# Optimization experiments

Measured on AMD Instinct MI355X. Metric: run time of the kernel, lower is better.

## Reference

```python
import jax, jax.numpy as jnp
import numpy as np

K = 9
SIGMA = 4.0
RADIUS = 16  # round(4*sigma)
IMAGE_SHAPE = (256, 256)


def _gaussian_kernel_1d():
    i = jnp.arange(2 * RADIUS + 1, dtype=jnp.float32) - RADIUS
    g = jnp.exp(-(i ** 2) / (2.0 * SIGMA ** 2))
    return g / jnp.sum(g)


def _gaussian_blur(x):
    # x: [b, H, W, 1]; separable Gaussian blur, reflect-101 borders (cv2 default)
    g = _gaussian_kernel_1d()
    xp = jnp.pad(x, ((0, 0), (RADIUS, RADIUS), (RADIUS, RADIUS), (0, 0)), mode='reflect')
    dn = ('NHWC', 'HWIO', 'NHWC')
    kv = g.reshape(2 * RADIUS + 1, 1, 1, 1)  # vertical pass
    kh = g.reshape(1, 2 * RADIUS + 1, 1, 1)  # horizontal pass
    y = jax.lax.conv_general_dilated(xp, kv, (1, 1), 'VALID', dimension_numbers=dn)
    y = jax.lax.conv_general_dilated(y, kh, (1, 1), 'VALID', dimension_numbers=dn)
    return y


def setup_inputs() -> dict:
    key = jax.random.key(0)
    k1, k2 = jax.random.split(key)
    inputs = jax.random.normal(k1, (8, 32, 32, 512), dtype=jnp.float32)
    feature_vector = jax.random.normal(k2, (16384, 512), dtype=jnp.float32)
    return {"inputs": inputs, "feature_vector": feature_vector}


def reference(inputs, feature_vector):
    b, h, w, c = inputs.shape
    feat = inputs.reshape(b * h * w, c)
    # pairwise euclidean distances: [b*h*w, N]
    d2 = (jnp.sum(feat ** 2, axis=-1, keepdims=True)
          + jnp.sum(feature_vector ** 2, axis=-1)[None, :]
          - 2.0 * feat @ feature_vector.T)
    dist = jnp.sqrt(jnp.maximum(d2, 0.0))
    # k smallest distances, ascending (equivalent to tf.sort(...)[..., :k])
    neg_topk, _ = jax.lax.top_k(-dist, K)
    score = -neg_topk  # [b*h*w, K], ascending
    mask = score[:, 0].reshape(b, h, w, 1)
    score = score.reshape(b, h * w, K)
    # patch with maximal nearest-neighbor distance
    idx = jnp.argmax(score[..., 0], axis=-1)  # [b]
    conf = jnp.take_along_axis(score, idx[:, None, None], axis=1)[:, 0, :]  # [b, K]
    exp_conf = jnp.exp(conf)
    weight = 1.0 - jnp.max(exp_conf, axis=-1) / jnp.sum(exp_conf, axis=-1)
    score_out = (jnp.max(score[..., 0], axis=-1) * weight)[:, None]  # [b, 1]
    mask = jax.image.resize(mask, (b, *IMAGE_SHAPE, 1), method='bilinear', antialias=False)
    mask = _gaussian_blur(mask)
    return score_out, mask
```

## Files before the change

kernel.cpp:

```cpp
#include <hip/hip_runtime.h>

typedef __attribute__((ext_vector_type(8))) short bf16x8;
typedef __attribute__((ext_vector_type(4))) float f32x4;

static constexpr int M = 8192;
static constexpr int N = 16384;
static constexpr int K = 512;
static constexpr int BM = 128;
static constexpr int BN = 128;
static constexpr int BK = 64;
static constexpr int KCHUNKS = K / BK;
static constexpr int NGROUPS_S = 8;
static constexpr int GROUP_N_S = N / NGROUPS_S;
static constexpr int NTILES_S = GROUP_N_S / BN;
static constexpr int NGROUPS_F = 16;
static constexpr int GROUP_N_F = N / NGROUPS_F;
static constexpr int NTILES_F = GROUP_N_F / BN;
static constexpr int NCHUNK = NTILES_F * KCHUNKS;
static constexpr float F_INF = 3.0e38f;

__device__ __forceinline__ unsigned short f2bf(float f) {
    unsigned int u = __float_as_uint(f);
    return (unsigned short)((u + 0x7fffu + ((u >> 16) & 1u)) >> 16);
}

__device__ __forceinline__ void gl_lds16(const unsigned short* g, unsigned short* l) {
    __builtin_amdgcn_global_load_lds(
        (const __attribute__((address_space(1))) unsigned int*)g,
        (__attribute__((address_space(3))) unsigned int*)l, 16, 0, 0);
}

__global__ void k_prep(const float* __restrict__ Q, const float* __restrict__ F,
                       unsigned short* __restrict__ Qb, unsigned short* __restrict__ Fb,
                       float* __restrict__ qn, float* __restrict__ fn) {
    int wid = blockIdx.x * 4 + (threadIdx.x >> 6);
    int lane = threadIdx.x & 63;
    bool isQ = wid < M;
    const float* src = isQ ? (Q + (size_t)wid * K) : (F + (size_t)(wid - M) * K);
    unsigned short* dst = isQ ? (Qb + (size_t)wid * K) : (Fb + (size_t)(wid - M) * K);
    const float4* p = reinterpret_cast<const float4*>(src) + lane * 2;
    float4 a = p[0], b = p[1];
    float s = a.x*a.x + a.y*a.y + a.z*a.z + a.w*a.w
            + b.x*b.x + b.y*b.y + b.z*b.z + b.w*b.w;
    bf16x8 v;
    v[0]=(short)f2bf(a.x); v[1]=(short)f2bf(a.y); v[2]=(short)f2bf(a.z); v[3]=(short)f2bf(a.w);
    v[4]=(short)f2bf(b.x); v[5]=(short)f2bf(b.y); v[6]=(short)f2bf(b.z); v[7]=(short)f2bf(b.w);
    *reinterpret_cast<bf16x8*>(dst + lane * 8) = v;
    #pragma unroll
    for (int d = 1; d < 64; d <<= 1) s += __shfl_xor(s, d);
    if (lane == 0) { if (isQ) qn[wid] = s; else fn[wid - M] = s; }
}

__global__ void k_norms(const float* __restrict__ Q, const float* __restrict__ F,
                        float* __restrict__ qn, float* __restrict__ fn) {
    int wid = blockIdx.x * 4 + (threadIdx.x >> 6);
    int lane = threadIdx.x & 63;
    const float* src = (wid < M) ? (Q + (size_t)wid * K) : (F + (size_t)(wid - M) * K);
    const float4* p = reinterpret_cast<const float4*>(src) + lane * 2;
    float4 a = p[0], b = p[1];
    float s = a.x*a.x + a.y*a.y + a.z*a.z + a.w*a.w
            + b.x*b.x + b.y*b.y + b.z*b.z + b.w*b.w;
    #pragma unroll
    for (int d = 1; d < 64; d <<= 1) s += __shfl_xor(s, d);
    if (lane == 0) { if (wid < M) qn[wid] = s; else fn[wid - M] = s; }
}

__global__ __launch_bounds__(256, 2)
void k_mingemm2(const unsigned short* __restrict__ Qb, const unsigned short* __restrict__ Fb,
                const float* __restrict__ qn, const float* __restrict__ fn,
                float* __restrict__ pv, unsigned int* __restrict__ pi) {
    __shared__ unsigned short As[2][BM * BK];
    __shared__ unsigned short Bs[2][BN * BK];
    __shared__ float qn_t[BM];
    __shared__ float fn_g[GROUP_N_F];

    const int tid = threadIdx.x;
    const int lane = tid & 63;
    const int wave = tid >> 6;
    const int wr = wave >> 1, wc = wave & 1;
    const int l15 = lane & 15, l4 = lane >> 4;

    const int wg = blockIdx.x;
    const int swz = (wg & 7) * 128 + (wg >> 3);
    const int group = swz >> 6;
    const int rowblk = swz & 63;
    const int row0 = rowblk * BM;
    const int gbase = group * GROUP_N_F;

    const int r_l = lane >> 3, p8 = lane & 7;
    const int g8 = p8 ^ r_l;
    const unsigned short* gA[4];
    const unsigned short* gB[4];
    #pragma unroll
    for (int i = 0; i < 4; ++i) {
        int row = (wave * 4 + i) * 8 + r_l;
        gA[i] = Qb + (size_t)(row0 + row) * K + g8 * 8;
        gB[i] = Fb + (size_t)(gbase + row) * K + g8 * 8;
    }

    auto stage = [&](int ct, int buf) {
        const int kc = ct & 7;
        const size_t bo = (size_t)(ct >> 3) * BN * K;
        #pragma unroll
        for (int i = 0; i < 4; ++i) gl_lds16(gA[i] + kc * BK, &As[buf][(wave * 4 + i) * 512]);
        #pragma unroll
        for (int i = 0; i < 4; ++i) gl_lds16(gB[i] + bo + kc * BK, &Bs[buf][(wave * 4 + i) * 512]);
    };

    for (int i = tid; i < GROUP_N_F; i += 256) fn_g[i] = fn[gbase + i];
    if (tid < BM) qn_t[tid] = qn[row0 + tid];
    stage(0, 0);
    __syncthreads();

    float qnv[4][4];
    #pragma unroll
    for (int fi = 0; fi < 4; ++fi)
        #pragma unroll
        for (int j = 0; j < 4; ++j)
            qnv[fi][j] = qn_t[wr*64 + fi*16 + l4*4 + j];

    float mval[4][4];
    unsigned int midx[4][4];
    #pragma unroll
    for (int a = 0; a < 4; ++a)
        #pragma unroll
        for (int b = 0; b < 4; ++b) { mval[a][b] = F_INF; midx[a][b] = 0; }

    int cur = 0;
    for (int nt = 0; nt < NTILES_F; ++nt) {
        f32x4 acc[4][4];
        #pragma unroll
        for (int a = 0; a < 4; ++a)
            #pragma unroll
            for (int b = 0; b < 4; ++b) acc[a][b] = f32x4{0.f, 0.f, 0.f, 0.f};

        for (int kc = 0; kc < KCHUNKS; ++kc) {
            const int ct = nt * KCHUNKS + kc;
            if (ct + 1 < NCHUNK) {
                stage(ct + 1, cur ^ 1);
                asm volatile("s_waitcnt vmcnt(8)" ::: "memory");
            } else {
                asm volatile("s_waitcnt vmcnt(0)" ::: "memory");
            }
            __builtin_amdgcn_sched_barrier(0);
            __builtin_amdgcn_s_barrier();
            #pragma unroll
            for (int ks = 0; ks < 2; ++ks) {
                const int gidx = ks * 4 + l4;
                bf16x8 af[4], bfv[4];
                #pragma unroll
                for (int fi = 0; fi < 4; ++fi) {
                    int r = wr*64 + fi*16 + l15;
                    int pg = gidx ^ (r & 7);
                    af[fi] = *reinterpret_cast<const bf16x8*>(&As[cur][r*BK + pg*8]);
                }
                #pragma unroll
                for (int fj = 0; fj < 4; ++fj) {
                    int r = wc*64 + fj*16 + l15;
                    int pg = gidx ^ (r & 7);
                    bfv[fj] = *reinterpret_cast<const bf16x8*>(&Bs[cur][r*BK + pg*8]);
                }
                #pragma unroll
                for (int fi = 0; fi < 4; ++fi)
                    #pragma unroll
                    for (int fj = 0; fj < 4; ++fj)
                        acc[fi][fj] = __builtin_amdgcn_mfma_f32_16x16x32_bf16(
                            af[fi], bfv[fj], acc[fi][fj], 0, 0, 0);
            }
            __builtin_amdgcn_sched_barrier(0);
            __builtin_amdgcn_s_barrier();
            cur ^= 1;
        }
        const int colb = gbase + nt * BN + wc * 64;
        float fnv[4];
        #pragma unroll
        for (int fj = 0; fj < 4; ++fj) fnv[fj] = fn_g[nt*BN + wc*64 + fj*16 + l15];
        #pragma unroll
        for (int fi = 0; fi < 4; ++fi) {
            #pragma unroll
            for (int j = 0; j < 4; ++j) {
                float qv = qnv[fi][j];
                #pragma unroll
                for (int fj = 0; fj < 4; ++fj) {
                    float d2 = qv + fnv[fj] - 2.0f * acc[fi][fj][j];
                    if (d2 < mval[fi][j]) {
                        mval[fi][j] = d2;
                        midx[fi][j] = (unsigned int)(colb + fj*16 + l15);
                    }
                }
            }
        }
    }
    #pragma unroll
    for (int fi = 0; fi < 4; ++fi) {
        #pragma unroll
        for (int j = 0; j < 4; ++j) {
            float v = mval[fi][j];
            unsigned int ix = midx[fi][j];
            #pragma unroll
            for (int d = 1; d < 16; d <<= 1) {
                float ov = __shfl_xor(v, d);
                unsigned int oi = (unsigned int)__shfl_xor((int)ix, d);
                if (ov < v) { v = ov; ix = oi; }
            }
            if (l15 == 0) {
                int rg = row0 + wr*64 + fi*16 + l4*4 + j;
                int pidx = rg * 32 + group*2 + wc;
                pv[pidx] = v;
                pi[pidx] = ix;
            }
        }
    }
}

__global__ __launch_bounds__(256, 2)
void k_mingemm_cast(const float* __restrict__ Q, const float* __restrict__ F,
                    const float* __restrict__ qn, const float* __restrict__ fn,
                    float* __restrict__ pv, unsigned int* __restrict__ pi) {
    __shared__ unsigned short As[BM * BK];
    __shared__ unsigned short Bs[BN * BK];
    __shared__ float qn_t[BM];
    __shared__ float fn_t[BN];

    const int tid = threadIdx.x;
    const int lane = tid & 63;
    const int wave = tid >> 6;
    const int wr = wave >> 1, wc = wave & 1;
    const int l15 = lane & 15, l4 = lane >> 4;

    const int row0 = blockIdx.x * BM;
    const int gbase = blockIdx.y * GROUP_N_S;

    const int srow = tid >> 3;
    const int p8 = tid & 7;
    const int g8 = p8 ^ (srow & 7);
    const float* pA[4];
    const float* pB[4];
    int dstOff[4];
    #pragma unroll
    for (int i = 0; i < 4; ++i) {
        int r = i * 32 + srow;
        pA[i] = Q + (size_t)(row0 + r) * K + g8 * 8;
        pB[i] = F + (size_t)(gbase + r) * K + g8 * 8;
        dstOff[i] = r * BK + p8 * 8;
    }

    float mval[4][4];
    unsigned int midx[4][4];
    float qnv[4][4];
    #pragma unroll
    for (int a = 0; a < 4; ++a)
        #pragma unroll
        for (int b = 0; b < 4; ++b) { mval[a][b] = F_INF; midx[a][b] = 0; qnv[a][b] = 0.f; }

    for (int nt = 0; nt < NTILES_S; ++nt) {
        f32x4 acc[4][4];
        #pragma unroll
        for (int a = 0; a < 4; ++a)
            #pragma unroll
            for (int b = 0; b < 4; ++b) acc[a][b] = f32x4{0.f, 0.f, 0.f, 0.f};

        for (int kc = 0; kc < KCHUNKS; ++kc) {
            __syncthreads();
            #pragma unroll
            for (int i = 0; i < 4; ++i) {
                const float4* sa = reinterpret_cast<const float4*>(pA[i] + kc * BK);
                float4 xa = sa[0], ya = sa[1];
                const float4* sb = reinterpret_cast<const float4*>(pB[i] + nt * (BN * K) + kc * BK);
                float4 xb = sb[0], yb = sb[1];
                bf16x8 va, vb;
                va[0]=(short)f2bf(xa.x); va[1]=(short)f2bf(xa.y); va[2]=(short)f2bf(xa.z); va[3]=(short)f2bf(xa.w);
                va[4]=(short)f2bf(ya.x); va[5]=(short)f2bf(ya.y); va[6]=(short)f2bf(ya.z); va[7]=(short)f2bf(ya.w);
                vb[0]=(short)f2bf(xb.x); vb[1]=(short)f2bf(xb.y); vb[2]=(short)f2bf(xb.z); vb[3]=(short)f2bf(xb.w);
                vb[4]=(short)f2bf(yb.x); vb[5]=(short)f2bf(yb.y); vb[6]=(short)f2bf(yb.z); vb[7]=(short)f2bf(yb.w);
                *reinterpret_cast<bf16x8*>(&As[dstOff[i]]) = va;
                *reinterpret_cast<bf16x8*>(&Bs[dstOff[i]]) = vb;
            }
            if (kc == 0) {
                if (nt == 0 && tid < BM) qn_t[tid] = qn[row0 + tid];
                if (tid < BN) fn_t[tid] = fn[gbase + nt * BN + tid];
            }
            __syncthreads();
            if (nt == 0 && kc == 0) {
                #pragma unroll
                for (int fi = 0; fi < 4; ++fi)
                    #pragma unroll
                    for (int j = 0; j < 4; ++j)
                        qnv[fi][j] = qn_t[wr*64 + fi*16 + l4*4 + j];
            }
            #pragma unroll
            for (int ks = 0; ks < 2; ++ks) {
                const int gidx = ks * 4 + l4;
                bf16x8 af[4], bfv[4];
                #pragma unroll
                for (int fi = 0; fi < 4; ++fi) {
                    int r = wr*64 + fi*16 + l15;
                    int pg = gidx ^ (r & 7);
                    af[fi] = *reinterpret_cast<const bf16x8*>(&As[r*BK + pg*8]);
                }
                #pragma unroll
                for (int fj = 0; fj < 4; ++fj) {
                    int r = wc*64 + fj*16 + l15;
                    int pg = gidx ^ (r & 7);
                    bfv[fj] = *reinterpret_cast<const bf16x8*>(&Bs[r*BK + pg*8]);
                }
                #pragma unroll
                for (int fi = 0; fi < 4; ++fi)
                    #pragma unroll
                    for (int fj = 0; fj < 4; ++fj)
                        acc[fi][fj] = __builtin_amdgcn_mfma_f32_16x16x32_bf16(
                            af[fi], bfv[fj], acc[fi][fj], 0, 0, 0);
            }
        }
        const int colb = gbase + nt * BN + wc * 64;
        float fnv[4];
        #pragma unroll
        for (int fj = 0; fj < 4; ++fj) fnv[fj] = fn_t[wc*64 + fj*16 + l15];
        #pragma unroll
        for (int fi = 0; fi < 4; ++fi) {
            #pragma unroll
            for (int j = 0; j < 4; ++j) {
                float qv = qnv[fi][j];
                #pragma unroll
                for (int fj = 0; fj < 4; ++fj) {
                    float d2 = qv + fnv[fj] - 2.0f * acc[fi][fj][j];
                    if (d2 < mval[fi][j]) {
                        mval[fi][j] = d2;
                        midx[fi][j] = (unsigned int)(colb + fj*16 + l15);
                    }
                }
            }
        }
    }
    #pragma unroll
    for (int fi = 0; fi < 4; ++fi) {
        #pragma unroll
        for (int j = 0; j < 4; ++j) {
            float v = mval[fi][j];
            unsigned int ix = midx[fi][j];
            #pragma unroll
            for (int d = 1; d < 16; d <<= 1) {
                float ov = __shfl_xor(v, d);
                unsigned int oi = (unsigned int)__shfl_xor((int)ix, d);
                if (ov < v) { v = ov; ix = oi; }
            }
            if (l15 == 0) {
                int rg = row0 + wr*64 + fi*16 + l4*4 + j;
                int pidx = rg * 16 + blockIdx.y * 2 + wc;
                pv[pidx] = v;
                pi[pidx] = ix;
            }
        }
    }
}

__global__ void k_refine(const float* __restrict__ Q, const float* __restrict__ F,
                         const float* __restrict__ pv, const unsigned int* __restrict__ pi,
                         float* __restrict__ minD, int PS) {
    int row = blockIdx.x * 4 + (threadIdx.x >> 6);
    int lane = threadIdx.x & 63;
    float v = F_INF; unsigned int ix = 0;
    if (lane < PS) { v = pv[row*PS + lane]; ix = pi[row*PS + lane]; }
    #pragma unroll
    for (int d = 1; d < 64; d <<= 1) {
        float ov = __shfl_xor(v, d);
        unsigned int oi = (unsigned int)__shfl_xor((int)ix, d);
        if (ov < v) { v = ov; ix = oi; }
    }
    const float4* q = reinterpret_cast<const float4*>(Q + (size_t)row * K) + lane*2;
    const float4* f = reinterpret_cast<const float4*>(F + (size_t)ix * K) + lane*2;
    float4 a0 = q[0], a1 = q[1], b0 = f[0], b1 = f[1];
    float s = 0.f, dx;
    dx = a0.x-b0.x; s += dx*dx;  dx = a0.y-b0.y; s += dx*dx;
    dx = a0.z-b0.z; s += dx*dx;  dx = a0.w-b0.w; s += dx*dx;
    dx = a1.x-b1.x; s += dx*dx;  dx = a1.y-b1.y; s += dx*dx;
    dx = a1.z-b1.z; s += dx*dx;  dx = a1.w-b1.w; s += dx*dx;
    #pragma unroll
    for (int d = 1; d < 64; d <<= 1) s += __shfl_xor(s, d);
    if (lane == 0) minD[row] = sqrtf(s);
}

__global__ void k_argmax(const float* __restrict__ minD, unsigned int* __restrict__ sel) {
    __shared__ float sv[256];
    __shared__ int si[256];
    int b = blockIdx.x, tid = threadIdx.x;
    float bv = -F_INF; int bi = 0;
    for (int p = tid; p < 1024; p += 256) {
        float v = minD[b*1024 + p];
        if (v > bv) { bv = v; bi = p; }
    }
    sv[tid] = bv; si[tid] = bi;
    __syncthreads();
    for (int s = 128; s > 0; s >>= 1) {
        if (tid < s) {
            if (sv[tid+s] > sv[tid] || (sv[tid+s] == sv[tid] && si[tid+s] < si[tid])) {
                sv[tid] = sv[tid+s]; si[tid] = si[tid+s];
            }
        }
        __syncthreads();
    }
    if (tid == 0) sel[b] = (unsigned int)(b*1024 + si[0]);
}

__global__ void k_dist8(const float* __restrict__ Q, const float* __restrict__ F,
                        const unsigned int* __restrict__ sel, float* __restrict__ d2all) {
    __shared__ float qs[8][512];
    int tid = threadIdx.x;
    int lane = tid & 63, wave = tid >> 6;
    for (int i = tid; i < 8*512; i += 256) {
        int b = i >> 9;
        qs[b][i & 511] = Q[(size_t)sel[b] * K + (i & 511)];
    }
    __syncthreads();
    int base = blockIdx.x * 128 + wave * 32;
    for (int r = 0; r < 32; ++r) {
        int row = base + r;
        const float4* fp = reinterpret_cast<const float4*>(F + (size_t)row * K) + lane*2;
        float4 f0 = fp[0], f1 = fp[1];
        float fv[8] = {f0.x,f0.y,f0.z,f0.w,f1.x,f1.y,f1.z,f1.w};
        float accb[8];
        #pragma unroll
        for (int b = 0; b < 8; ++b) {
            float s = 0.f;
            #pragma unroll
            for (int e = 0; e < 8; ++e) {
                float d = fv[e] - qs[b][lane*8 + e];
                s += d * d;
            }
            accb[b] = s;
        }
        #pragma unroll
        for (int d = 1; d < 64; d <<= 1)
            #pragma unroll
            for (int b = 0; b < 8; ++b) accb[b] += __shfl_xor(accb[b], d);
        if (lane == 0) {
            #pragma unroll
            for (int b = 0; b < 8; ++b) d2all[b * N + row] = accb[b];
        }
    }
}

__global__ void k_sel9(const float* __restrict__ d2all, float* __restrict__ out) {
    __shared__ float sv[256 * 10];
    int b = blockIdx.x, tid = threadIdx.x;
    float v[9];
    #pragma unroll
    for (int i = 0; i < 9; ++i) v[i] = F_INF;
    for (int i = tid; i < N; i += 256) {
        float x = d2all[b * N + i];
        #pragma unroll
        for (int s = 0; s < 9; ++s) {
            float lo = fminf(v[s], x), hi = fmaxf(v[s], x);
            v[s] = lo; x = hi;
        }
    }
    #pragma unroll
    for (int i = 0; i < 9; ++i) sv[tid*10 + i] = v[i];
    sv[tid*10 + 9] = F_INF;
    __syncthreads();
    for (int s = 128; s > 0; s >>= 1) {
        if (tid < s) {
            int ia = 1, ib = 1;
            float av = sv[tid*10], bv = sv[(tid+s)*10];
            float c[9];
            #pragma unroll
            for (int k = 0; k < 9; ++k) {
                bool ta = av <= bv;
                c[k] = ta ? av : bv;
                float na = sv[tid*10 + ia], nb = sv[(tid+s)*10 + ib];
                if (ta) { av = na; ++ia; } else { bv = nb; ++ib; }
            }
            #pragma unroll
            for (int k = 0; k < 9; ++k) sv[tid*10 + k] = c[k];
        }
        __syncthreads();
    }
    if (tid == 0) {
        float c[9];
        #pragma unroll
        for (int i = 0; i < 9; ++i) c[i] = sqrtf(fmaxf(sv[i], 0.f));
        float S = 0.f;
        #pragma unroll
        for (int i = 0; i < 9; ++i) S += expf(c[i] - c[8]);
        out[b] = c[0] * (1.f - 1.f / S);
    }
}

__global__ void k_top9(const float* __restrict__ Q, const float* __restrict__ F,
                       const unsigned int* __restrict__ sel, float* __restrict__ part9) {
    __shared__ float qs[512];
    __shared__ float dist[2048];
    __shared__ float rv[256];
    __shared__ int ri[256];
    int b = blockIdx.x >> 3, g = blockIdx.x & 7;
    int tid = threadIdx.x;
    unsigned int srow = sel[b];
    if (tid < 128)
        reinterpret_cast<float4*>(qs)[tid] =
            reinterpret_cast<const float4*>(Q + (size_t)srow * K)[tid];
    __syncthreads();
    #pragma unroll
    for (int e = 0; e < 8; ++e) {
        int fl = tid + 256*e;
        const float* fp = F + (size_t)(g*2048 + fl) * K;
        float s = 0.f;
        for (int k = 0; k < 512; k += 4) {
            float4 fv4 = *reinterpret_cast<const float4*>(fp + k);
            float d0 = qs[k]   - fv4.x;
            float d1 = qs[k+1] - fv4.y;
            float d2 = qs[k+2] - fv4.z;
            float d3 = qs[k+3] - fv4.w;
            s += d0*d0 + d1*d1 + d2*d2 + d3*d3;
        }
        dist[fl] = s;
    }
    __syncthreads();
    for (int it = 0; it < 9; ++it) {
        float lv = F_INF; int li = 0;
        #pragma unroll
        for (int e = 0; e < 8; ++e) {
            int idx = tid + 256*e;
            float v = dist[idx];
            if (v < lv) { lv = v; li = idx; }
        }
        rv[tid] = lv; ri[tid] = li;
        __syncthreads();
        for (int s = 128; s > 0; s >>= 1) {
            if (tid < s && rv[tid+s] < rv[tid]) { rv[tid] = rv[tid+s]; ri[tid] = ri[tid+s]; }
            __syncthreads();
        }
        if (tid == 0) {
            part9[(b*8+g)*9 + it] = rv[0];
            dist[ri[0]] = F_INF;
        }
        __syncthreads();
    }
}

__global__ void k_final(const float* __restrict__ part9, float* __restrict__ out) {
    int b = threadIdx.x;
    if (b >= 8) return;
    float arr[9];
    #pragma unroll
    for (int i = 0; i < 9; ++i) arr[i] = F_INF;
    for (int g = 0; g < 8; ++g)
        for (int i = 0; i < 9; ++i) {
            float v = part9[(b*8+g)*9 + i];
            #pragma unroll
            for (int s = 0; s < 9; ++s) {
                float lo = fminf(arr[s], v), hi = fmaxf(arr[s], v);
                arr[s] = lo; v = hi;
            }
        }
    float c[9];
    #pragma unroll
    for (int i = 0; i < 9; ++i) c[i] = sqrtf(fmaxf(arr[i], 0.f));
    float c8 = c[8], S = 0.f;
    #pragma unroll
    for (int i = 0; i < 9; ++i) S += expf(c[i] - c8);
    float w = 1.f - 1.f / S;
    out[b] = c[0] * w;
}

__global__ void k_wmat(float* __restrict__ W) {
    int idx = blockIdx.x * 256 + threadIdx.x;
    int o = idx >> 5, j = idx & 31;
    float gsum = 0.f;
    #pragma unroll
    for (int u = 0; u < 33; ++u) { float d = (float)(u - 16); gsum += expf(-d*d * (1.f/32.f)); }
    float acc = 0.f;
    for (int u = 0; u < 33; ++u) {
        float d = (float)(u - 16);
        float gu = expf(-d*d * (1.f/32.f));
        int y = o + u - 16;
        y = y < 0 ? -y : (y > 255 ? 510 - y : y);
        float xin = ((float)y + 0.5f) * 0.125f - 0.5f;
        float j0f = floorf(xin);
        int j0 = (int)j0f;
        float wfr = xin - j0f;
        float r;
        if (j0 < 0) r = (j == 0) ? 1.f : 0.f;
        else if (j0 >= 31) r = (j == 31) ? 1.f : 0.f;
        else r = (j == j0) ? (1.f - wfr) : ((j == j0 + 1) ? wfr : 0.f);
        acc += gu * r;
    }
    W[idx] = acc / gsum;
}

__global__ void k_mask(const float* __restrict__ minD, const float* __restrict__ W,
                       float* __restrict__ outm) {
    __shared__ float Ms[1024];
    __shared__ float Ws[8192];
    __shared__ float Ts[8192];
    int b = blockIdx.x, tid = threadIdx.x;
    for (int i = tid; i < 1024; i += 256) Ms[i] = minD[b*1024 + i];
    for (int i = tid; i < 8192; i += 256) Ws[i] = W[i];
    __syncthreads();
    {
        int o = tid;
        float wrow[32];
        #pragma unroll
        for (int i = 0; i < 32; ++i) wrow[i] = Ws[o*32 + i];
        for (int j = 0; j < 32; ++j) {
            float s = 0.f;
            #pragma unroll
            for (int i = 0; i < 32; ++i) s += wrow[i] * Ms[i*32 + j];
            Ts[o*32 + j] = s;
        }
    }
    __syncthreads();
    {
        int p = tid;
        float wp[32];
        #pragma unroll
        for (int j = 0; j < 32; ++j) wp[j] = Ws[p*32 + j];
        float* dst = outm + (size_t)b * 65536;
        for (int o = 0; o < 256; ++o) {
            float s = 0.f;
            #pragma unroll
            for (int j = 0; j < 32; ++j) s += Ts[o*32 + j] * wp[j];
            dst[o*256 + p] = s;
        }
    }
}

extern "C" void kernel_launch(void* const* d_in, const int* in_sizes, int n_in,
                              void* d_out, int out_size, void* d_ws, size_t ws_size,
                              hipStream_t stream) {
    const float* Q = (const float*)d_in[0];
    const float* F = (const float*)d_in[1];
    float* out = (float*)d_out;

    const size_t smallFloats = (size_t)8192*32*2 + 8192 + 8 + 576 + (size_t)8*N + 8192 + 16384 + 8192;
    const size_t REQ = smallFloats*4 + (size_t)M*K*2 + (size_t)N*K*2;
    const bool fast = ws_size >= REQ;
    const int PS = fast ? 32 : 16;

    float* ws = (float*)d_ws;
    float* pv = ws;
    unsigned int* pi = (unsigned int*)(pv + 8192*PS);
    float* minD = (float*)(pi + 8192*PS);
    unsigned int* sel = (unsigned int*)(minD + 8192);
    float* part9 = (float*)(sel + 8);
    float* d2all = part9 + 576;
    float* qn = d2all + (size_t)8*N;
    float* fn = qn + 8192;
    float* W  = fn + 16384;
    unsigned short* Qb = (unsigned short*)(W + 8192);
    unsigned short* Fb = Qb + (size_t)M*K;

    k_wmat <<<dim3(32), 256, 0, stream>>>(W);
    if (fast) {
        k_prep <<<dim3((M + N) / 4), 256, 0, stream>>>(Q, F, Qb, Fb, qn, fn);
        k_mingemm2<<<dim3(M / BM * NGROUPS_F), 256, 0, stream>>>(Qb, Fb, qn, fn, pv, pi);
        k_refine<<<dim3(M / 4), 256, 0, stream>>>(Q, F, pv, pi, minD, PS);
        k_argmax<<<dim3(8), 256, 0, stream>>>(minD, sel);
        k_dist8<<<dim3(N / 128), 256, 0, stream>>>(Q, F, sel, d2all);
        k_sel9 <<<dim3(8), 256, 0, stream>>>(d2all, out);
    } else {
        k_norms<<<dim3((M + N) / 4), 256, 0, stream>>>(Q, F, qn, fn);
        k_mingemm_cast<<<dim3(M / BM, NGROUPS_S), 256, 0, stream>>>(Q, F, qn, fn, pv, pi);
        k_refine<<<dim3(M / 4), 256, 0, stream>>>(Q, F, pv, pi, minD, PS);
        k_argmax<<<dim3(8), 256, 0, stream>>>(minD, sel);
        k_top9 <<<dim3(64), 256, 0, stream>>>(Q, F, sel, part9);
        k_final<<<dim3(1), 64, 0, stream>>>(part9, out);
    }
    k_mask <<<dim3(8), 256, 0, stream>>>(minD, W, out + 8);
}
```

Measured before the change: 346.4 us.

## Replace min-GEMM with 256x256 output-tile kernel using 8 waves and interleaved LDS loads

The fast path's min-distance GEMM moves from 128x128 tiles that each loop over a group of N columns to one 256x256 output tile per workgroup with 512 threads. Each workgroup covers a single column block and writes a per-row partial min for it, so there are 64 partials per row and k_refine reads all of them. Inside the kernel, MFMAs on the first half of the A fragments are interleaved with LDS reads of the second half and with the global-to-LDS prefetch, and s_setprio raises priority around the MFMA bursts. The aim is more arithmetic per byte staged and better overlap of memory with compute, at the cost of more registers, a larger partial-min buffer and a cross-wave reduction through LDS.

```diff
diff --git a/kernel.cpp b/kernel.cpp
--- a/kernel.cpp
+++ b/kernel.cpp
@@ -6,17 +6,17 @@
 static constexpr int M = 8192;
 static constexpr int N = 16384;
 static constexpr int K = 512;
-static constexpr int BM = 128;
-static constexpr int BN = 128;
+static constexpr int BM = 256;
+static constexpr int BN = 256;
 static constexpr int BK = 64;
 static constexpr int KCHUNKS = K / BK;
+static constexpr int RBLK = M / BM;
+static constexpr int CBLK = N / BN;
+static constexpr int BMs = 128;
+static constexpr int BKs = 64;
 static constexpr int NGROUPS_S = 8;
 static constexpr int GROUP_N_S = N / NGROUPS_S;
-static constexpr int NTILES_S = GROUP_N_S / BN;
-static constexpr int NGROUPS_F = 16;
-static constexpr int GROUP_N_F = N / NGROUPS_F;
-static constexpr int NTILES_F = GROUP_N_F / BN;
-static constexpr int NCHUNK = NTILES_F * KCHUNKS;
+static constexpr int NTILES_S = GROUP_N_S / 128;
 static constexpr float F_INF = 3.0e38f;
 
 __device__ __forceinline__ unsigned short f2bf(float f) {
@@ -65,14 +65,167 @@
     if (lane == 0) { if (wid < M) qn[wid] = s; else fn[wid - M] = s; }
 }
 
-__global__ __launch_bounds__(256, 2)
-void k_mingemm2(const unsigned short* __restrict__ Qb, const unsigned short* __restrict__ Fb,
+__global__ __launch_bounds__(512, 2)
+void k_mingemm3(const unsigned short* __restrict__ Qb, const unsigned short* __restrict__ Fb,
                 const float* __restrict__ qn, const float* __restrict__ fn,
                 float* __restrict__ pv, unsigned int* __restrict__ pi) {
     __shared__ unsigned short As[2][BM * BK];
     __shared__ unsigned short Bs[2][BN * BK];
-    __shared__ float qn_t[BM];
-    __shared__ float fn_g[GROUP_N_F];
+    __shared__ float redv[BM][4];
+    __shared__ unsigned int redi[BM][4];
+
+    const int tid = threadIdx.x;
+    const int lane = tid & 63;
+    const int wave = tid >> 6;
+    const int wr = wave >> 2;
+    const int wc = wave & 3;
+    const int l15 = lane & 15, l4 = lane >> 4;
+
+    const int wg = blockIdx.x;
+    const int x = wg & 7, q = wg >> 3;
+    const int c_blk = x * 8 + (q & 7);
+    const int r_blk = q >> 3;
+    const int row0 = r_blk * BM;
+    const int col0 = c_blk * BN;
+
+    const int r_l = lane >> 3, p8 = lane & 7;
+    const int g8 = p8 ^ r_l;
+    const unsigned short* gA[4];
+    const unsigned short* gB[4];
+    #pragma unroll
+    for (int i = 0; i < 4; ++i) {
+        int row = wave * 32 + i * 8 + r_l;
+        gA[i] = Qb + (size_t)(row0 + row) * K + g8 * 8;
+        gB[i] = Fb + (size_t)(col0 + row) * K + g8 * 8;
+    }
+
+    auto stage = [&](int kc, int buf) {
+        #pragma unroll
+        for (int i = 0; i < 4; ++i) gl_lds16(gA[i] + kc * BK, &As[buf][(wave*32 + i*8) * BK]);
+        #pragma unroll
+        for (int i = 0; i < 4; ++i) gl_lds16(gB[i] + kc * BK, &Bs[buf][(wave*32 + i*8) * BK]);
+    };
+
+    f32x4 acc[8][4];
+    #pragma unroll
+    for (int a = 0; a < 8; ++a)
+        #pragma unroll
+        for (int b = 0; b < 4; ++b) acc[a][b] = f32x4{0.f, 0.f, 0.f, 0.f};
+
+    stage(0, 0);
+    stage(1, 1);
+    asm volatile("s_waitcnt vmcnt(8)" ::: "memory");
+    __builtin_amdgcn_sched_barrier(0);
+    __builtin_amdgcn_s_barrier();
+
+    for (int kc = 0; kc < KCHUNKS; ++kc) {
+        const int p = kc & 1;
+        bf16x8 af[4][2], bfv[4][2];
+        #pragma unroll
+        for (int ks = 0; ks < 2; ++ks) {
+            const int gidx = ks * 4 + l4;
+            #pragma unroll
+            for (int fi = 0; fi < 4; ++fi) {
+                int r = wr*128 + fi*16 + l15;
+                int pg = gidx ^ (r & 7);
+                af[fi][ks] = *reinterpret_cast<const bf16x8*>(&As[p][r*BK + pg*8]);
+            }
+            #pragma unroll
+            for (int fj = 0; fj < 4; ++fj) {
+                int r = wc*64 + fj*16 + l15;
+                int pg = gidx ^ (r & 7);
+                bfv[fj][ks] = *reinterpret_cast<const bf16x8*>(&Bs[p][r*BK + pg*8]);
+            }
+        }
+        __builtin_amdgcn_s_setprio(1);
+        #pragma unroll
+        for (int ks = 0; ks < 2; ++ks)
+            #pragma unroll
+            for (int fi = 0; fi < 4; ++fi)
+                #pragma unroll
+                for (int fj = 0; fj < 4; ++fj)
+                    acc[fi][fj] = __builtin_amdgcn_mfma_f32_16x16x32_bf16(
+                        af[fi][ks], bfv[fj][ks], acc[fi][fj], 0, 0, 0);
+        __builtin_amdgcn_s_setprio(0);
+        bf16x8 ah[4][2];
+        #pragma unroll
+        for (int ks = 0; ks < 2; ++ks) {
+            const int gidx = ks * 4 + l4;
+            #pragma unroll
+            for (int fi = 0; fi < 4; ++fi) {
+                int r = wr*128 + 64 + fi*16 + l15;
+                int pg = gidx ^ (r & 7);
+                ah[fi][ks] = *reinterpret_cast<const bf16x8*>(&As[p][r*BK + pg*8]);
+            }
+        }
+        asm volatile("s_waitcnt lgkmcnt(0)" ::: "memory");
+        __builtin_amdgcn_sched_barrier(0);
+        __builtin_amdgcn_s_barrier();
+        if (kc + 2 < KCHUNKS) {
+            stage(kc + 2, p);
+            asm volatile("s_waitcnt vmcnt(8)" ::: "memory");
+        } else {
+            asm volatile("s_waitcnt vmcnt(0)" ::: "memory");
+        }
+        __builtin_amdgcn_sched_barrier(0);
+        __builtin_amdgcn_s_barrier();
+        __builtin_amdgcn_s_setprio(1);
+        #pragma unroll
+        for (int ks = 0; ks < 2; ++ks)
+            #pragma unroll
+            for (int fi = 0; fi < 4; ++fi)
+                #pragma unroll
+                for (int fj = 0; fj < 4; ++fj)
+                    acc[4+fi][fj] = __builtin_amdgcn_mfma_f32_16x16x32_bf16(
+                        ah[fi][ks], bfv[fj][ks], acc[4+fi][fj], 0, 0, 0);
+        __builtin_amdgcn_s_setprio(0);
+    }
+
+    float fnv[4];
+    #pragma unroll
+    for (int fj = 0; fj < 4; ++fj) fnv[fj] = fn[col0 + wc*64 + fj*16 + l15];
+    #pragma unroll
+    for (int fi = 0; fi < 8; ++fi) {
+        #pragma unroll
+        for (int j = 0; j < 4; ++j) {
+            int rloc = wr*128 + fi*16 + l4*4 + j;
+            float qv = qn[row0 + rloc];
+            float v = F_INF; unsigned int ix = 0;
+            #pragma unroll
+            for (int fj = 0; fj < 4; ++fj) {
+                float d2 = qv + fnv[fj] - 2.0f * acc[fi][fj][j];
+                if (d2 < v) { v = d2; ix = (unsigned int)(col0 + wc*64 + fj*16 + l15); }
+            }
+            #pragma unroll
+            for (int d = 1; d < 16; d <<= 1) {
+                float ov = __shfl_xor(v, d);
+                unsigned int oi = (unsigned int)__shfl_xor((int)ix, d);
+                if (ov < v) { v = ov; ix = oi; }
+            }
+            if (l15 == 0) { redv[rloc][wc] = v; redi[rloc][wc] = ix; }
+        }
+    }
+    __syncthreads();
+    if (tid < BM) {
+        float v = redv[tid][0]; unsigned int ix = redi[tid][0];
+        #pragma unroll
+        for (int w2 = 1; w2 < 4; ++w2) {
+            float ov = redv[tid][w2];
+            if (ov < v) { v = ov; ix = redi[tid][w2]; }
+        }
+        pv[(size_t)(row0 + tid) * CBLK + c_blk] = v;
+        pi[(size_t)(row0 + tid) * CBLK + c_blk] = ix;
+    }
+}
+
+__global__ __launch_bounds__(256, 2)
+void k_mingemm_cast(const float* __restrict__ Q, const float* __restrict__ F,
+                    const float* __restrict__ qn, const float* __restrict__ fn,
+                    float* __restrict__ pv, unsigned int* __restrict__ pi) {
+    __shared__ unsigned short As[BMs * BKs];
+    __shared__ unsigned short Bs[BMs * BKs];
+    __shared__ float qn_t[BMs];
+    __shared__ float fn_t[BMs];
 
     const int tid = threadIdx.x;
     const int lane = tid & 63;
@@ -80,54 +233,32 @@
     const int wr = wave >> 1, wc = wave & 1;
     const int l15 = lane & 15, l4 = lane >> 4;
 
-    const int wg = blockIdx.x;
-    const int swz = (wg & 7) * 128 + (wg >> 3);
-    const int group = swz >> 6;
-    const int rowblk = swz & 63;
-    const int row0 = rowblk * BM;
-    const int gbase = group * GROUP_N_F;
-
-    const int r_l = lane >> 3, p8 = lane & 7;
-    const int g8 = p8 ^ r_l;
-    const unsigned short* gA[4];
-    const unsigned short* gB[4];
+    const int row0 = blockIdx.x * BMs;
+    const int gbase = blockIdx.y * GROUP_N_S;
+
+    const int srow = tid >> 3;
+    const int p8 = tid & 7;
+    const int g8 = p8 ^ (srow & 7);
+    const float* pA[4];
+    const float* pB[4];
+    int dstOff[4];
     #pragma unroll
     for (int i = 0; i < 4; ++i) {
-        int row = (wave * 4 + i) * 8 + r_l;
-        gA[i] = Qb + (size_t)(row0 + row) * K + g8 * 8;
-        gB[i] = Fb + (size_t)(gbase + row) * K + g8 * 8;
-    }
-
-    auto stage = [&](int ct, int buf) {
-        const int kc = ct & 7;
-        const size_t bo = (size_t)(ct >> 3) * BN * K;
-        #pragma unroll
-        for (int i = 0; i < 4; ++i) gl_lds16(gA[i] + kc * BK, &As[buf][(wave * 4 + i) * 512]);
-        #pragma unroll
-        for (int i = 0; i < 4; ++i) gl_lds16(gB[i] + bo + kc * BK, &Bs[buf][(wave * 4 + i) * 512]);
-    };
-
-    for (int i = tid; i < GROUP_N_F; i += 256) fn_g[i] = fn[gbase + i];
-    if (tid < BM) qn_t[tid] = qn[row0 + tid];
-    stage(0, 0);
-    __syncthreads();
-
-    float qnv[4][4];
-    #pragma unroll
-    for (int fi = 0; fi < 4; ++fi)
-        #pragma unroll
-        for (int j = 0; j < 4; ++j)
-            qnv[fi][j] = qn_t[wr*64 + fi*16 + l4*4 + j];
+        int r = i * 32 + srow;
+        pA[i] = Q + (size_t)(row0 + r) * K + g8 * 8;
+        pB[i] = F + (size_t)(gbase + r) * K + g8 * 8;
+        dstOff[i] = r * BKs + p8 * 8;
+    }
 
     float mval[4][4];
     unsigned int midx[4][4];
+    float qnv[4][4];
     #pragma unroll
     for (int a = 0; a < 4; ++a)
         #pragma unroll
-        for (int b = 0; b < 4; ++b) { mval[a][b] = F_INF; midx[a][b] = 0; }
-
-    int cur = 0;
-    for (int nt = 0; nt < NTILES_F; ++nt) {
+        for (int b = 0; b < 4; ++b) { mval[a][b] = F_INF; midx[a][b] = 0; qnv[a][b] = 0.f; }
+
+    for (int nt = 0; nt < NTILES_S; ++nt) {
         f32x4 acc[4][4];
         #pragma unroll
         for (int a = 0; a < 4; ++a)
@@ -135,15 +266,33 @@
             for (int b = 0; b < 4; ++b) acc[a][b] = f32x4{0.f, 0.f, 0.f, 0.f};
 
         for (int kc = 0; kc < KCHUNKS; ++kc) {
-            const int ct = nt * KCHUNKS + kc;
-            if (ct + 1 < NCHUNK) {
-                stage(ct + 1, cur ^ 1);
-                asm volatile("s_waitcnt vmcnt(8)" ::: "memory");
-            } else {
-                asm volatile("s_waitcnt vmcnt(0)" ::: "memory");
-            }
-            __builtin_amdgcn_sched_barrier(0);
-            __builtin_amdgcn_s_barrier();
+            __syncthreads();
+            #pragma unroll
+            for (int i = 0; i < 4; ++i) {
+                const float4* sa = reinterpret_cast<const float4*>(pA[i] + kc * BKs);
+                float4 xa = sa[0], ya = sa[1];
+                const float4* sb = reinterpret_cast<const float4*>(pB[i] + nt * (128 * K) + kc * BKs);
+                float4 xb = sb[0], yb = sb[1];
+                bf16x8 va, vb;
+                va[0]=(short)f2bf(xa.x); va[1]=(short)f2bf(xa.y); va[2]=(short)f2bf(xa.z); va[3]=(short)f2bf(xa.w);
+                va[4]=(short)f2bf(ya.x); va[5]=(short)f2bf(ya.y); va[6]=(short)f2bf(ya.z); va[7]=(short)f2bf(ya.w);
+                vb[0]=(short)f2bf(xb.x); vb[1]=(short)f2bf(xb.y); vb[2]=(short)f2bf(xb.z); vb[3]=(short)f2bf(xb.w);
+                vb[4]=(short)f2bf(yb.x); vb[5]=(short)f2bf(yb.y); vb[6]=(short)f2bf(yb.z); vb[7]=(short)f2bf(yb.w);
+                *reinterpret_cast<bf16x8*>(&As[dstOff[i]]) = va;
+                *reinterpret_cast<bf16x8*>(&Bs[dstOff[i]]) = vb;
+            }
+            if (kc == 0) {
+                if (nt == 0 && tid < BMs) qn_t[tid] = qn[row0 + tid];
+                if (tid < 128) fn_t[tid] = fn[gbase + nt * 128 + tid];
+            }
+            __syncthreads();
+            if (nt == 0 && kc == 0) {
+                #pragma unroll
+                for (int fi = 0; fi < 4; ++fi)
+                    #pragma unroll
+                    for (int j = 0; j < 4; ++j)
+                        qnv[fi][j] = qn_t[wr*64 + fi*16 + l4*4 + j];
+            }
             #pragma unroll
             for (int ks = 0; ks < 2; ++ks) {
                 const int gidx = ks * 4 + l4;
@@ -152,13 +301,13 @@
                 for (int fi = 0; fi < 4; ++fi) {
                     int r = wr*64 + fi*16 + l15;
                     int pg = gidx ^ (r & 7);
-                    af[fi] = *reinterpret_cast<const bf16x8*>(&As[cur][r*BK + pg*8]);
+                    af[fi] = *reinterpret_cast<const bf16x8*>(&As[r*BKs + pg*8]);
                 }
                 #pragma unroll
                 for (int fj = 0; fj < 4; ++fj) {
                     int r = wc*64 + fj*16 + l15;
                     int pg = gidx ^ (r & 7);
-                    bfv[fj] = *reinterpret_cast<const bf16x8*>(&Bs[cur][r*BK + pg*8]);
+                    bfv[fj] = *reinterpret_cast<const bf16x8*>(&Bs[r*BKs + pg*8]);
                 }
                 #pragma unroll
                 for (int fi = 0; fi < 4; ++fi)
@@ -167,14 +316,11 @@
                         acc[fi][fj] = __builtin_amdgcn_mfma_f32_16x16x32_bf16(
                             af[fi], bfv[fj], acc[fi][fj], 0, 0, 0);
             }
-            __builtin_amdgcn_sched_barrier(0);
-            __builtin_amdgcn_s_barrier();
-            cur ^= 1;
-        }
-        const int colb = gbase + nt * BN + wc * 64;
+        }
+        const int colb = gbase + nt * 128 + wc * 64;
         float fnv[4];
         #pragma unroll
-        for (int fj = 0; fj < 4; ++fj) fnv[fj] = fn_g[nt*BN + wc*64 + fj*16 + l15];
+        for (int fj = 0; fj < 4; ++fj) fnv[fj] = fn_t[wc*64 + fj*16 + l15];
         #pragma unroll
         for (int fi = 0; fi < 4; ++fi) {
             #pragma unroll
@@ -205,147 +351,6 @@
             }
             if (l15 == 0) {
                 int rg = row0 + wr*64 + fi*16 + l4*4 + j;
-                int pidx = rg * 32 + group*2 + wc;
-                pv[pidx] = v;
-                pi[pidx] = ix;
-            }
-        }
-    }
-}
-
-__global__ __launch_bounds__(256, 2)
-void k_mingemm_cast(const float* __restrict__ Q, const float* __restrict__ F,
-                    const float* __restrict__ qn, const float* __restrict__ fn,
-                    float* __restrict__ pv, unsigned int* __restrict__ pi) {
-    __shared__ unsigned short As[BM * BK];
-    __shared__ unsigned short Bs[BN * BK];
-    __shared__ float qn_t[BM];
-    __shared__ float fn_t[BN];
-
-    const int tid = threadIdx.x;
-    const int lane = tid & 63;
-    const int wave = tid >> 6;
-    const int wr = wave >> 1, wc = wave & 1;
-    const int l15 = lane & 15, l4 = lane >> 4;
-
-    const int row0 = blockIdx.x * BM;
-    const int gbase = blockIdx.y * GROUP_N_S;
-
-    const int srow = tid >> 3;
-    const int p8 = tid & 7;
-    const int g8 = p8 ^ (srow & 7);
-    const float* pA[4];
-    const float* pB[4];
-    int dstOff[4];
-    #pragma unroll
-    for (int i = 0; i < 4; ++i) {
-        int r = i * 32 + srow;
-        pA[i] = Q + (size_t)(row0 + r) * K + g8 * 8;
-        pB[i] = F + (size_t)(gbase + r) * K + g8 * 8;
-        dstOff[i] = r * BK + p8 * 8;
-    }
-
-    float mval[4][4];
-    unsigned int midx[4][4];
-    float qnv[4][4];
-    #pragma unroll
-    for (int a = 0; a < 4; ++a)
-        #pragma unroll
-        for (int b = 0; b < 4; ++b) { mval[a][b] = F_INF; midx[a][b] = 0; qnv[a][b] = 0.f; }
-
-    for (int nt = 0; nt < NTILES_S; ++nt) {
-        f32x4 acc[4][4];
-        #pragma unroll
-        for (int a = 0; a < 4; ++a)
-            #pragma unroll
-            for (int b = 0; b < 4; ++b) acc[a][b] = f32x4{0.f, 0.f, 0.f, 0.f};
-
-        for (int kc = 0; kc < KCHUNKS; ++kc) {
-            __syncthreads();
-            #pragma unroll
-            for (int i = 0; i < 4; ++i) {
-                const float4* sa = reinterpret_cast<const float4*>(pA[i] + kc * BK);
-                float4 xa = sa[0], ya = sa[1];
-                const float4* sb = reinterpret_cast<const float4*>(pB[i] + nt * (BN * K) + kc * BK);
-                float4 xb = sb[0], yb = sb[1];
-                bf16x8 va, vb;
-                va[0]=(short)f2bf(xa.x); va[1]=(short)f2bf(xa.y); va[2]=(short)f2bf(xa.z); va[3]=(short)f2bf(xa.w);
-                va[4]=(short)f2bf(ya.x); va[5]=(short)f2bf(ya.y); va[6]=(short)f2bf(ya.z); va[7]=(short)f2bf(ya.w);
-                vb[0]=(short)f2bf(xb.x); vb[1]=(short)f2bf(xb.y); vb[2]=(short)f2bf(xb.z); vb[3]=(short)f2bf(xb.w);
-                vb[4]=(short)f2bf(yb.x); vb[5]=(short)f2bf(yb.y); vb[6]=(short)f2bf(yb.z); vb[7]=(short)f2bf(yb.w);
-                *reinterpret_cast<bf16x8*>(&As[dstOff[i]]) = va;
-                *reinterpret_cast<bf16x8*>(&Bs[dstOff[i]]) = vb;
-            }
-            if (kc == 0) {
-                if (nt == 0 && tid < BM) qn_t[tid] = qn[row0 + tid];
-                if (tid < BN) fn_t[tid] = fn[gbase + nt * BN + tid];
-            }
-            __syncthreads();
-            if (nt == 0 && kc == 0) {
-                #pragma unroll
-                for (int fi = 0; fi < 4; ++fi)
-                    #pragma unroll
-                    for (int j = 0; j < 4; ++j)
-                        qnv[fi][j] = qn_t[wr*64 + fi*16 + l4*4 + j];
-            }
-            #pragma unroll
-            for (int ks = 0; ks < 2; ++ks) {
-                const int gidx = ks * 4 + l4;
-                bf16x8 af[4], bfv[4];
-                #pragma unroll
-                for (int fi = 0; fi < 4; ++fi) {
-                    int r = wr*64 + fi*16 + l15;
-                    int pg = gidx ^ (r & 7);
-                    af[fi] = *reinterpret_cast<const bf16x8*>(&As[r*BK + pg*8]);
-                }
-                #pragma unroll
-                for (int fj = 0; fj < 4; ++fj) {
-                    int r = wc*64 + fj*16 + l15;
-                    int pg = gidx ^ (r & 7);
-                    bfv[fj] = *reinterpret_cast<const bf16x8*>(&Bs[r*BK + pg*8]);
-                }
-                #pragma unroll
-                for (int fi = 0; fi < 4; ++fi)
-                    #pragma unroll
-                    for (int fj = 0; fj < 4; ++fj)
-                        acc[fi][fj] = __builtin_amdgcn_mfma_f32_16x16x32_bf16(
-                            af[fi], bfv[fj], acc[fi][fj], 0, 0, 0);
-            }
-        }
-        const int colb = gbase + nt * BN + wc * 64;
-        float fnv[4];
-        #pragma unroll
-        for (int fj = 0; fj < 4; ++fj) fnv[fj] = fn_t[wc*64 + fj*16 + l15];
-        #pragma unroll
-        for (int fi = 0; fi < 4; ++fi) {
-            #pragma unroll
-            for (int j = 0; j < 4; ++j) {
-                float qv = qnv[fi][j];
-                #pragma unroll
-                for (int fj = 0; fj < 4; ++fj) {
-                    float d2 = qv + fnv[fj] - 2.0f * acc[fi][fj][j];
-                    if (d2 < mval[fi][j]) {
-                        mval[fi][j] = d2;
-                        midx[fi][j] = (unsigned int)(colb + fj*16 + l15);
-                    }
-                }
-            }
-        }
-    }
-    #pragma unroll
-    for (int fi = 0; fi < 4; ++fi) {
-        #pragma unroll
-        for (int j = 0; j < 4; ++j) {
-            float v = mval[fi][j];
-            unsigned int ix = midx[fi][j];
-            #pragma unroll
-            for (int d = 1; d < 16; d <<= 1) {
-                float ov = __shfl_xor(v, d);
-                unsigned int oi = (unsigned int)__shfl_xor((int)ix, d);
-                if (ov < v) { v = ov; ix = oi; }
-            }
-            if (l15 == 0) {
-                int rg = row0 + wr*64 + fi*16 + l4*4 + j;
                 int pidx = rg * 16 + blockIdx.y * 2 + wc;
                 pv[pidx] = v;
                 pi[pidx] = ix;
@@ -360,7 +365,7 @@
     int row = blockIdx.x * 4 + (threadIdx.x >> 6);
     int lane = threadIdx.x & 63;
     float v = F_INF; unsigned int ix = 0;
-    if (lane < PS) { v = pv[row*PS + lane]; ix = pi[row*PS + lane]; }
+    if (lane < PS) { v = pv[(size_t)row*PS + lane]; ix = pi[(size_t)row*PS + lane]; }
     #pragma unroll
     for (int d = 1; d < 64; d <<= 1) {
         float ov = __shfl_xor(v, d);
@@ -631,15 +636,15 @@
     const float* F = (const float*)d_in[1];
     float* out = (float*)d_out;
 
-    const size_t smallFloats = (size_t)8192*32*2 + 8192 + 8 + 576 + (size_t)8*N + 8192 + 16384 + 8192;
+    const size_t smallFloats = (size_t)8192*64*2 + 8192 + 8 + 576 + (size_t)8*N + 8192 + 16384 + 8192;
     const size_t REQ = smallFloats*4 + (size_t)M*K*2 + (size_t)N*K*2;
     const bool fast = ws_size >= REQ;
-    const int PS = fast ? 32 : 16;
+    const int PS = fast ? 64 : 16;
 
     float* ws = (float*)d_ws;
     float* pv = ws;
-    unsigned int* pi = (unsigned int*)(pv + 8192*PS);
-    float* minD = (float*)(pi + 8192*PS);
+    unsigned int* pi = (unsigned int*)(pv + 8192*64);
+    float* minD = (float*)(pi + 8192*64);
     unsigned int* sel = (unsigned int*)(minD + 8192);
     float* part9 = (float*)(sel + 8);
     float* d2all = part9 + 576;
@@ -652,14 +657,14 @@
     k_wmat <<<dim3(32), 256, 0, stream>>>(W);
     if (fast) {
         k_prep <<<dim3((M + N) / 4), 256, 0, stream>>>(Q, F, Qb, Fb, qn, fn);
-        k_mingemm2<<<dim3(M / BM * NGROUPS_F), 256, 0, stream>>>(Qb, Fb, qn, fn, pv, pi);
+        k_mingemm3<<<dim3(RBLK * CBLK), 512, 0, stream>>>(Qb, Fb, qn, fn, pv, pi);
         k_refine<<<dim3(M / 4), 256, 0, stream>>>(Q, F, pv, pi, minD, PS);
         k_argmax<<<dim3(8), 256, 0, stream>>>(minD, sel);
         k_dist8<<<dim3(N / 128), 256, 0, stream>>>(Q, F, sel, d2all);
         k_sel9 <<<dim3(8), 256, 0, stream>>>(d2all, out);
     } else {
         k_norms<<<dim3((M + N) / 4), 256, 0, stream>>>(Q, F, qn, fn);
-        k_mingemm_cast<<<dim3(M / BM, NGROUPS_S), 256, 0, stream>>>(Q, F, qn, fn, pv, pi);
+        k_mingemm_cast<<<dim3(M / BMs, NGROUPS_S), 256, 0, stream>>>(Q, F, qn, fn, pv, pi);
         k_refine<<<dim3(M / 4), 256, 0, stream>>>(Q, F, pv, pi, minD, PS);
         k_argmax<<<dim3(8), 256, 0, stream>>>(minD, sel);
         k_top9 <<<dim3(64), 256, 0, stream>>>(Q, F, sel, part9);
```

After: 346.7 us. Within noise of the previous version (+0.1%).
